# Kernel optimization log

Hardware: AMD Instinct MI355X
Metric: run time of the kernel (lower is better)

## Reference

```python
import jax, jax.numpy as jnp
import numpy as np

DIM = 256
HEADS = 8
DIM_HEAD = 64
INNER = HEADS * DIM_HEAD           # 512
DPG = DIM // HEADS                 # 32 in-channels per group (grouped conv)
EPS = 1e-5


def setup_inputs() -> dict:
    key = jax.random.key(0)
    ks = jax.random.split(key, 7)
    b, p, k = 4, 1024, 32
    x = jax.random.normal(ks[0], (b, p, k, DIM), dtype=jnp.float32)
    # BatchNorm2d affine params (torch default init: gamma=1, beta=0)
    bn_gamma = jnp.ones((DIM,), jnp.float32)
    bn_beta = jnp.zeros((DIM,), jnp.float32)
    # grouped 1x1 conv weights: per head maps DPG -> DIM_HEAD, shape [H, DIM_HEAD, DPG]
    Wq = jax.random.normal(ks[1], (HEADS, DIM_HEAD, DPG), jnp.float32) * 0.02
    Wk = jax.random.normal(ks[2], (HEADS, DIM_HEAD, DPG), jnp.float32) * 0.02
    Wv = jax.random.normal(ks[3], (HEADS, DIM_HEAD, DPG), jnp.float32) * 0.02
    # output Linear: y = x @ Wout + bout, Wout [INNER, DIM]
    Wout = jax.random.normal(ks[4], (INNER, DIM), jnp.float32) * 0.02
    bout = jnp.zeros((DIM,), jnp.float32)
    return {"x": x, "bn_gamma": bn_gamma, "bn_beta": bn_beta,
            "Wq": Wq, "Wk": Wk, "Wv": Wv, "Wout": Wout, "bout": bout}


def reference(x, bn_gamma, bn_beta, Wq, Wk, Wv, Wout, bout):
    b, p, k, d = x.shape
    scale = DIM_HEAD ** (-0.5)
    # BatchNorm2d in training mode: per-channel batch stats over (b, p, k)
    mean = jnp.mean(x, axis=(0, 1, 2))
    var = jnp.var(x, axis=(0, 1, 2))           # biased variance (torch BN normalization)
    xn = (x - mean) * jax.lax.rsqrt(var + EPS) * bn_gamma + bn_beta
    # grouped 1x1 conv projections: split channels into HEADS groups of DPG
    xg = xn.reshape(b, p, k, HEADS, DPG)       # [b,p,k,h,c]
    q = jnp.einsum('bpkhc,hoc->bphko', xg, Wq)  # [b,p,h,k,dim_head]
    kk = jnp.einsum('bpkhc,hoc->bphko', xg, Wk)
    v = jnp.einsum('bpkhc,hoc->bphko', xg, Wv)
    # attention over neighbors within each point
    dots = jnp.einsum('bphid,bphjd->bphij', q, kk) * scale  # [b,p,h,k,k]
    attn = jax.nn.softmax(dots, axis=-1)
    out = jnp.einsum('bphij,bphjd->bphid', attn, v)         # [b,p,h,k,dim_head]
    out = out.transpose(0, 1, 3, 2, 4).reshape(b, p, k, INNER)  # b p k (h d)
    return out @ Wout + bout                   # [b,p,k,dim]
```

## Files before the change

### kernel.cpp

```cpp
#include <hip/hip_runtime.h>
#include <hip/hip_bf16.h>

#define DIM    256
#define HEADS  8
#define DH     64
#define DPG    32
#define KNB    32
#define INNER  512
#define EPS    1e-5f

#define WS_SUMB 0
#define WS_SSQB 1024
#define WS_WF   2048
#define WS_QB   26624
#define WS_WT   28160

typedef float f32x4  __attribute__((ext_vector_type(4)));
typedef short bf16x8 __attribute__((ext_vector_type(8)));

__device__ __forceinline__ unsigned short f2bf(float f){
    unsigned u = __float_as_uint(f);
    u += 0x7fffu + ((u >> 16) & 1u);
    return (unsigned short)(u >> 16);
}
__device__ __forceinline__ unsigned packbf(float a, float b){
    union { __hip_bfloat162 h; unsigned u; } c;
    c.h = __float22bfloat162_rn(make_float2(a, b));
    return c.u;
}
__device__ __forceinline__ bf16x8 pack8(f32x4 a, f32x4 b){
    union { unsigned u[4]; bf16x8 v; } r;
    r.u[0] = packbf(a[0], a[1]); r.u[1] = packbf(a[2], a[3]);
    r.u[2] = packbf(b[0], b[1]); r.u[3] = packbf(b[2], b[3]);
    return r.v;
}

#define QKSWZ(row, col) ((row) * 64 + ((col) ^ ((((row) ^ ((row) >> 2)) & 7) << 3)))
#define AOSWZ(row, col) ((row) * 512 + ((col) ^ (((row) & 7) << 3)))

__global__ __launch_bounds__(256) void bn_stats_k(const f32x4* __restrict__ x4,
                                                  float* __restrict__ ws, int n4) {
    __shared__ f32x4 rs[4][64], rss[4][64];
    const int tid = blockIdx.x * 256 + threadIdx.x;
    const int stride = gridDim.x * 256;
    f32x4 s  = {0.f, 0.f, 0.f, 0.f};
    f32x4 ss = {0.f, 0.f, 0.f, 0.f};
    int f = tid;
    const int nloop = n4 / (4 * stride);
    for (int i = 0; i < nloop; ++i) {
        f32x4 v0 = x4[f];
        f32x4 v1 = x4[f + stride];
        f32x4 v2 = x4[f + 2 * stride];
        f32x4 v3 = x4[f + 3 * stride];
        f += 4 * stride;
        s += v0; ss += v0 * v0;
        s += v1; ss += v1 * v1;
        s += v2; ss += v2 * v2;
        s += v3; ss += v3 * v3;
    }
    for (; f < n4; f += stride) { f32x4 v = x4[f]; s += v; ss += v * v; }
    int c4 = threadIdx.x & 63, wv = threadIdx.x >> 6;
    rs[wv][c4] = s; rss[wv][c4] = ss;
    __syncthreads();
    const float* rsf  = (const float*)rs;
    const float* rssf = (const float*)rss;
    int ch = threadIdx.x;
    float S = rsf[ch]  + rsf[256 + ch]  + rsf[512 + ch]  + rsf[768 + ch];
    float Q = rssf[ch] + rssf[256 + ch] + rssf[512 + ch] + rssf[768 + ch];
    int bank = (blockIdx.x & 3) * 256;
    atomicAdd(&ws[WS_SUMB + bank + ch], S);
    atomicAdd(&ws[WS_SSQB + bank + ch], Q);
}

__global__ __launch_bounds__(256) void wt_k(const float* __restrict__ Wout, float* __restrict__ ws) {
    __shared__ unsigned short tile[64][65];
    const int k0 = blockIdx.x * 64, n0 = blockIdx.y * 64;
    const int t = threadIdx.x;
    #pragma unroll
    for (int i = 0; i < 16; ++i) {
        int e = t + 256 * i;
        int kk = e >> 6, nn = e & 63;
        tile[kk][nn] = f2bf(Wout[(k0 + kk) * DIM + n0 + nn]);
    }
    __syncthreads();
    unsigned short* wt = (unsigned short*)(ws + WS_WT);
    #pragma unroll
    for (int i = 0; i < 2; ++i) {
        int f = t + 256 * i;
        int nn = f >> 3, kc = f & 7;
        union { unsigned short s[8]; uint4 u; } pk;
        #pragma unroll
        for (int j = 0; j < 8; ++j) pk.s[j] = tile[kc * 8 + j][nn];
        *(uint4*)(wt + (size_t)(n0 + nn) * INNER + k0 + kc * 8) = pk.u;
    }
}

__global__ __launch_bounds__(256) void fold_k(const float* __restrict__ Wq,
                                              const float* __restrict__ Wk,
                                              const float* __restrict__ Wv,
                                              const float* __restrict__ gam,
                                              const float* __restrict__ bet,
                                              float* __restrict__ ws, float inv_n) {
    __shared__ float wl[64][33];
    __shared__ float scs[DPG], shs[DPG];
    const int m = blockIdx.x, h = blockIdx.y, t = threadIdx.x;
    const float* W = (m == 0 ? Wq : (m == 1 ? Wk : Wv)) + h * DH * DPG;
    if (t < DPG) {
        int c = h * DPG + t;
        float S = ws[WS_SUMB + c] + ws[WS_SUMB + 256 + c] + ws[WS_SUMB + 512 + c] + ws[WS_SUMB + 768 + c];
        float Q = ws[WS_SSQB + c] + ws[WS_SSQB + 256 + c] + ws[WS_SSQB + 512 + c] + ws[WS_SSQB + 768 + c];
        float mean = S * inv_n;
        float var  = Q * inv_n - mean * mean;
        float sc   = gam[c] * rsqrtf(var + EPS);
        scs[t] = sc;
        shs[t] = bet[c] - mean * sc;
    }
    #pragma unroll
    for (int i = 0; i < 8; ++i) {
        int e = t + 256 * i;
        wl[e >> 5][e & 31] = W[e];
    }
    __syncthreads();
    const float qsc = (m == 0) ? 0.125f : 1.f;
    unsigned short* wf = (unsigned short*)(ws + WS_WF) + (m * HEADS + h) * DH * DPG;
    {
        int o = t >> 2, c0 = (t & 3) * 8;
        union { unsigned short s[8]; uint4 u; } pk;
        #pragma unroll
        for (int j = 0; j < 8; ++j) pk.s[j] = f2bf(wl[o][c0 + j] * scs[c0 + j] * qsc);
        *(uint4*)(wf + o * DPG + c0) = pk.u;
    }
    if (t < DH) {
        float bias = 0.f;
        #pragma unroll
        for (int c = 0; c < DPG; ++c) bias += shs[c] * wl[t][c];
        ws[WS_QB + (m * HEADS + h) * DH + t] = bias * qsc;
    }
}

__global__ __launch_bounds__(256, 5) void attn_fused(const float* __restrict__ x,
                                                     const float* __restrict__ ws,
                                                     const float* __restrict__ bout,
                                                     float* __restrict__ out) {
    __shared__ __align__(16) unsigned short lds[16384];

    const int t = threadIdx.x;
    const int w = t >> 6, L = t & 63;
    const int lr = L & 15, g = L >> 4;
    const long long rb = (long long)blockIdx.x * KNB;

    unsigned short* qsm = lds + w * 2048;
    unsigned short* ksm = lds + 8192 + w * 2048;
    unsigned short* psm = qsm;
    unsigned short* vtm = ksm;
    const unsigned short* wfb = (const unsigned short*)(ws + WS_WF);
    const unsigned short* WT  = (const unsigned short*)(ws + WS_WT);

    bf16x8 xa[2][2];
    #pragma unroll
    for (int hs = 0; hs < 2; ++hs)
        #pragma unroll
        for (int it = 0; it < 2; ++it) {
            const float* xp = x + (rb + it * 16 + lr) * DIM + (w + hs * 4) * DPG + g * 8;
            xa[hs][it] = pack8(*(const f32x4*)xp, *(const f32x4*)(xp + 4));
        }

    f32x4 av[2][2][4];

    #pragma unroll
    for (int hs = 0; hs < 2; ++hs) {
        const int h = w + hs * 4;

        #pragma unroll
        for (int m = 0; m < 2; ++m) {
            unsigned short* dst = m ? ksm : qsm;
            #pragma unroll
            for (int ot = 0; ot < 4; ++ot) {
                const int o = ot * 16 + lr;
                bf16x8 wf = *(const bf16x8*)(wfb + ((m * HEADS + h) * DH + o) * DPG + g * 8);
                float bv = ws[WS_QB + (m * HEADS + h) * DH + o];
                #pragma unroll
                for (int it = 0; it < 2; ++it) {
                    f32x4 c = {bv, bv, bv, bv};
                    c = __builtin_amdgcn_mfma_f32_16x16x32_bf16(xa[hs][it], wf, c, 0, 0, 0);
                    unsigned u01 = packbf(c[0], c[1]);
                    unsigned u23 = packbf(c[2], c[3]);
                    const int r0 = it * 16 + g * 4;
                    dst[QKSWZ(r0 + 0, o)] = (unsigned short)u01;
                    dst[QKSWZ(r0 + 1, o)] = (unsigned short)(u01 >> 16);
                    dst[QKSWZ(r0 + 2, o)] = (unsigned short)u23;
                    dst[QKSWZ(r0 + 3, o)] = (unsigned short)(u23 >> 16);
                }
            }
        }

        f32x4 dt[2][2];
        #pragma unroll
        for (int it = 0; it < 2; ++it)
            #pragma unroll
            for (int jt = 0; jt < 2; ++jt) dt[it][jt] = (f32x4){0.f, 0.f, 0.f, 0.f};
        #pragma unroll
        for (int ksp = 0; ksp < 2; ++ksp) {
            bf16x8 qa[2], kb[2];
            #pragma unroll
            for (int it = 0; it < 2; ++it)
                qa[it] = *(const bf16x8*)(qsm + QKSWZ(it * 16 + lr, ksp * 32 + g * 8));
            #pragma unroll
            for (int jt = 0; jt < 2; ++jt)
                kb[jt] = *(const bf16x8*)(ksm + QKSWZ(jt * 16 + lr, ksp * 32 + g * 8));
            #pragma unroll
            for (int it = 0; it < 2; ++it)
                #pragma unroll
                for (int jt = 0; jt < 2; ++jt)
                    dt[it][jt] = __builtin_amdgcn_mfma_f32_16x16x32_bf16(qa[it], kb[jt], dt[it][jt], 0, 0, 0);
        }

        #pragma unroll
        for (int it = 0; it < 2; ++it)
            #pragma unroll
            for (int r = 0; r < 4; ++r) {
                float m0 = fmaxf(dt[it][0][r], dt[it][1][r]);
                m0 = fmaxf(m0, __shfl_xor(m0, 1, 64));
                m0 = fmaxf(m0, __shfl_xor(m0, 2, 64));
                m0 = fmaxf(m0, __shfl_xor(m0, 4, 64));
                m0 = fmaxf(m0, __shfl_xor(m0, 8, 64));
                float e0 = __expf(dt[it][0][r] - m0);
                float e1 = __expf(dt[it][1][r] - m0);
                float s = e0 + e1;
                s += __shfl_xor(s, 1, 64);
                s += __shfl_xor(s, 2, 64);
                s += __shfl_xor(s, 4, 64);
                s += __shfl_xor(s, 8, 64);
                float inv = 1.f / s;
                int row = it * 16 + g * 4 + r;
                unsigned up = packbf(e0 * inv, e1 * inv);
                psm[QKSWZ(row, lr)]      = (unsigned short)up;
                psm[QKSWZ(row, lr + 16)] = (unsigned short)(up >> 16);
            }

        #pragma unroll
        for (int ot = 0; ot < 4; ++ot) {
            const int o = ot * 16 + lr;
            bf16x8 wf = *(const bf16x8*)(wfb + ((2 * HEADS + h) * DH + o) * DPG + g * 8);
            float bv = ws[WS_QB + (2 * HEADS + h) * DH + o];
            #pragma unroll
            for (int it = 0; it < 2; ++it) {
                f32x4 c = {bv, bv, bv, bv};
                c = __builtin_amdgcn_mfma_f32_16x16x32_bf16(xa[hs][it], wf, c, 0, 0, 0);
                uint2 u;
                u.x = packbf(c[0], c[1]);
                u.y = packbf(c[2], c[3]);
                *(uint2*)(vtm + QKSWZ(o & 31, (o >> 5) * 32 + it * 16 + g * 4)) = u;
            }
        }

        #pragma unroll
        for (int it = 0; it < 2; ++it) {
            bf16x8 pa = *(const bf16x8*)(psm + QKSWZ(it * 16 + lr, g * 8));
            #pragma unroll
            for (int ot = 0; ot < 4; ++ot) {
                bf16x8 vb = *(const bf16x8*)(vtm + QKSWZ((ot & 1) * 16 + lr, (ot >> 1) * 32 + g * 8));
                f32x4 c = {0.f, 0.f, 0.f, 0.f};
                av[hs][it][ot] = __builtin_amdgcn_mfma_f32_16x16x32_bf16(pa, vb, c, 0, 0, 0);
            }
        }
    }

    __syncthreads();
    unsigned short* aos = lds;
    #pragma unroll
    for (int hs = 0; hs < 2; ++hs)
        #pragma unroll
        for (int it = 0; it < 2; ++it)
            #pragma unroll
            for (int ot = 0; ot < 4; ++ot)
                #pragma unroll
                for (int r = 0; r < 4; ++r)
                    aos[AOSWZ(it * 16 + g * 4 + r, (w + hs * 4) * 64 + ot * 16 + lr)]
                        = f2bf(av[hs][it][ot][r]);
    __syncthreads();

    f32x4 oacc[2][4];
    #pragma unroll
    for (int n4 = 0; n4 < 4; ++n4) {
        float bv = bout[(w * 4 + n4) * 16 + lr];
        oacc[0][n4] = (f32x4){bv, bv, bv, bv};
        oacc[1][n4] = (f32x4){bv, bv, bv, bv};
    }
    #pragma unroll 4
    for (int ksp = 0; ksp < 16; ++ksp) {
        bf16x8 a0 = *(const bf16x8*)(aos + AOSWZ(lr, ksp * 32 + g * 8));
        bf16x8 a1 = *(const bf16x8*)(aos + AOSWZ(16 + lr, ksp * 32 + g * 8));
        #pragma unroll
        for (int n4 = 0; n4 < 4; ++n4) {
            const int n = (w * 4 + n4) * 16 + lr;
            bf16x8 bvv = *(const bf16x8*)(WT + (size_t)n * INNER + ksp * 32 + g * 8);
            oacc[0][n4] = __builtin_amdgcn_mfma_f32_16x16x32_bf16(a0, bvv, oacc[0][n4], 0, 0, 0);
            oacc[1][n4] = __builtin_amdgcn_mfma_f32_16x16x32_bf16(a1, bvv, oacc[1][n4], 0, 0, 0);
        }
    }
    #pragma unroll
    for (int it = 0; it < 2; ++it)
        #pragma unroll
        for (int n4 = 0; n4 < 4; ++n4)
            #pragma unroll
            for (int r = 0; r < 4; ++r)
                out[(rb + it * 16 + g * 4 + r) * DIM + (w * 4 + n4) * 16 + lr] = oacc[it][n4][r];
}

extern "C" void kernel_launch(void* const* d_in, const int* in_sizes, int n_in,
                              void* d_out, int out_size, void* d_ws, size_t ws_size,
                              hipStream_t stream) {
    const float* x  = (const float*)d_in[0];
    const float* g  = (const float*)d_in[1];
    const float* b  = (const float*)d_in[2];
    const float* wq = (const float*)d_in[3];
    const float* wk = (const float*)d_in[4];
    const float* wv = (const float*)d_in[5];
    const float* wo = (const float*)d_in[6];
    const float* bo = (const float*)d_in[7];
    float* ws = (float*)d_ws;

    int rows = in_sizes[0] / DIM;
    int npts = rows / KNB;

    hipMemsetAsync(d_ws, 0, 8192, stream);
    wt_k<<<dim3(INNER / 64, DIM / 64), 256, 0, stream>>>(wo, ws);
    bn_stats_k<<<1024, 256, 0, stream>>>((const f32x4*)x, ws, rows * (DIM / 4));
    fold_k<<<dim3(3, HEADS), 256, 0, stream>>>(wq, wk, wv, g, b, ws, 1.0f / (float)rows);
    attn_fused<<<npts, 256, 0, stream>>>(x, ws, bo, (float*)d_out);
}
```

Before: 482.0 us.

## Merge weight transpose and BN stats kernels; pack AV outputs to bf16 early

```diff
diff --git a/kernel.cpp b/kernel.cpp
--- a/kernel.cpp
+++ b/kernel.cpp
@@ -38,60 +38,64 @@
 #define QKSWZ(row, col) ((row) * 64 + ((col) ^ ((((row) ^ ((row) >> 2)) & 7) << 3)))
 #define AOSWZ(row, col) ((row) * 512 + ((col) ^ (((row) & 7) << 3)))
 
-__global__ __launch_bounds__(256) void bn_stats_k(const f32x4* __restrict__ x4,
-                                                  float* __restrict__ ws, int n4) {
-    __shared__ f32x4 rs[4][64], rss[4][64];
-    const int tid = blockIdx.x * 256 + threadIdx.x;
-    const int stride = gridDim.x * 256;
-    f32x4 s  = {0.f, 0.f, 0.f, 0.f};
-    f32x4 ss = {0.f, 0.f, 0.f, 0.f};
-    int f = tid;
-    const int nloop = n4 / (4 * stride);
-    for (int i = 0; i < nloop; ++i) {
-        f32x4 v0 = x4[f];
-        f32x4 v1 = x4[f + stride];
-        f32x4 v2 = x4[f + 2 * stride];
-        f32x4 v3 = x4[f + 3 * stride];
-        f += 4 * stride;
-        s += v0; ss += v0 * v0;
-        s += v1; ss += v1 * v1;
-        s += v2; ss += v2 * v2;
-        s += v3; ss += v3 * v3;
-    }
-    for (; f < n4; f += stride) { f32x4 v = x4[f]; s += v; ss += v * v; }
-    int c4 = threadIdx.x & 63, wv = threadIdx.x >> 6;
-    rs[wv][c4] = s; rss[wv][c4] = ss;
-    __syncthreads();
-    const float* rsf  = (const float*)rs;
-    const float* rssf = (const float*)rss;
-    int ch = threadIdx.x;
-    float S = rsf[ch]  + rsf[256 + ch]  + rsf[512 + ch]  + rsf[768 + ch];
-    float Q = rssf[ch] + rssf[256 + ch] + rssf[512 + ch] + rssf[768 + ch];
-    int bank = (blockIdx.x & 3) * 256;
-    atomicAdd(&ws[WS_SUMB + bank + ch], S);
-    atomicAdd(&ws[WS_SSQB + bank + ch], Q);
-}
-
-__global__ __launch_bounds__(256) void wt_k(const float* __restrict__ Wout, float* __restrict__ ws) {
-    __shared__ unsigned short tile[64][65];
-    const int k0 = blockIdx.x * 64, n0 = blockIdx.y * 64;
+__global__ __launch_bounds__(256) void prep_k(const float* __restrict__ Wout,
+                                              const f32x4* __restrict__ x4,
+                                              float* __restrict__ ws, int n4) {
+    __shared__ __align__(16) unsigned char smem[8448];
     const int t = threadIdx.x;
-    #pragma unroll
-    for (int i = 0; i < 16; ++i) {
-        int e = t + 256 * i;
-        int kk = e >> 6, nn = e & 63;
-        tile[kk][nn] = f2bf(Wout[(k0 + kk) * DIM + n0 + nn]);
-    }
-    __syncthreads();
-    unsigned short* wt = (unsigned short*)(ws + WS_WT);
-    #pragma unroll
-    for (int i = 0; i < 2; ++i) {
-        int f = t + 256 * i;
-        int nn = f >> 3, kc = f & 7;
-        union { unsigned short s[8]; uint4 u; } pk;
-        #pragma unroll
-        for (int j = 0; j < 8; ++j) pk.s[j] = tile[kc * 8 + j][nn];
-        *(uint4*)(wt + (size_t)(n0 + nn) * INNER + k0 + kc * 8) = pk.u;
+    if (blockIdx.x < 32) {
+        unsigned short (*tile)[65] = (unsigned short (*)[65])smem;
+        const int k0 = (blockIdx.x & 7) * 64, n0 = (blockIdx.x >> 3) * 64;
+        #pragma unroll
+        for (int i = 0; i < 16; ++i) {
+            int e = t + 256 * i;
+            int kk = e >> 6, nn = e & 63;
+            tile[kk][nn] = f2bf(Wout[(k0 + kk) * DIM + n0 + nn]);
+        }
+        __syncthreads();
+        unsigned short* wt = (unsigned short*)(ws + WS_WT);
+        #pragma unroll
+        for (int i = 0; i < 2; ++i) {
+            int f = t + 256 * i;
+            int nn = f >> 3, kc = f & 7;
+            union { unsigned short s[8]; uint4 u; } pk;
+            #pragma unroll
+            for (int j = 0; j < 8; ++j) pk.s[j] = tile[kc * 8 + j][nn];
+            *(uint4*)(wt + (size_t)(n0 + nn) * INNER + k0 + kc * 8) = pk.u;
+        }
+    } else {
+        f32x4 (*rs)[64]  = (f32x4 (*)[64])smem;
+        f32x4 (*rss)[64] = (f32x4 (*)[64])(smem + 4096);
+        const int bid = blockIdx.x - 32;
+        const int tid = bid * 256 + t;
+        const int stride = 1024 * 256;
+        f32x4 s  = {0.f, 0.f, 0.f, 0.f};
+        f32x4 ss = {0.f, 0.f, 0.f, 0.f};
+        int f = tid;
+        const int nloop = n4 / (4 * stride);
+        for (int i = 0; i < nloop; ++i) {
+            f32x4 v0 = x4[f];
+            f32x4 v1 = x4[f + stride];
+            f32x4 v2 = x4[f + 2 * stride];
+            f32x4 v3 = x4[f + 3 * stride];
+            f += 4 * stride;
+            s += v0; ss += v0 * v0;
+            s += v1; ss += v1 * v1;
+            s += v2; ss += v2 * v2;
+            s += v3; ss += v3 * v3;
+        }
+        for (; f < n4; f += stride) { f32x4 v = x4[f]; s += v; ss += v * v; }
+        int c4 = t & 63, wv = t >> 6;
+        rs[wv][c4] = s; rss[wv][c4] = ss;
+        __syncthreads();
+        const float* rsf  = (const float*)rs;
+        const float* rssf = (const float*)rss;
+        int ch = t;
+        float S = rsf[ch]  + rsf[256 + ch]  + rsf[512 + ch]  + rsf[768 + ch];
+        float Q = rssf[ch] + rssf[256 + ch] + rssf[512 + ch] + rssf[768 + ch];
+        int bank = (bid & 3) * 256;
+        atomicAdd(&ws[WS_SUMB + bank + ch], S);
+        atomicAdd(&ws[WS_SSQB + bank + ch], Q);
     }
 }
 
@@ -138,7 +142,7 @@
     }
 }
 
-__global__ __launch_bounds__(256, 5) void attn_fused(const float* __restrict__ x,
+__global__ __launch_bounds__(256, 4) void attn_fused(const float* __restrict__ x,
                                                      const float* __restrict__ ws,
                                                      const float* __restrict__ bout,
                                                      float* __restrict__ out) {
@@ -165,7 +169,7 @@
             xa[hs][it] = pack8(*(const f32x4*)xp, *(const f32x4*)(xp + 4));
         }
 
-    f32x4 av[2][2][4];
+    unsigned av_pk[2][2][4][2];
 
     #pragma unroll
     for (int hs = 0; hs < 2; ++hs) {
@@ -261,7 +265,9 @@
             for (int ot = 0; ot < 4; ++ot) {
                 bf16x8 vb = *(const bf16x8*)(vtm + QKSWZ((ot & 1) * 16 + lr, (ot >> 1) * 32 + g * 8));
                 f32x4 c = {0.f, 0.f, 0.f, 0.f};
-                av[hs][it][ot] = __builtin_amdgcn_mfma_f32_16x16x32_bf16(pa, vb, c, 0, 0, 0);
+                c = __builtin_amdgcn_mfma_f32_16x16x32_bf16(pa, vb, c, 0, 0, 0);
+                av_pk[hs][it][ot][0] = packbf(c[0], c[1]);
+                av_pk[hs][it][ot][1] = packbf(c[2], c[3]);
             }
         }
     }
@@ -273,11 +279,16 @@
         #pragma unroll
         for (int it = 0; it < 2; ++it)
             #pragma unroll
-            for (int ot = 0; ot < 4; ++ot)
-                #pragma unroll
-                for (int r = 0; r < 4; ++r)
-                    aos[AOSWZ(it * 16 + g * 4 + r, (w + hs * 4) * 64 + ot * 16 + lr)]
-                        = f2bf(av[hs][it][ot][r]);
+            for (int ot = 0; ot < 4; ++ot) {
+                unsigned u0 = av_pk[hs][it][ot][0];
+                unsigned u1 = av_pk[hs][it][ot][1];
+                const int colb = (w + hs * 4) * 64 + ot * 16 + lr;
+                const int r0 = it * 16 + g * 4;
+                aos[AOSWZ(r0 + 0, colb)] = (unsigned short)u0;
+                aos[AOSWZ(r0 + 1, colb)] = (unsigned short)(u0 >> 16);
+                aos[AOSWZ(r0 + 2, colb)] = (unsigned short)u1;
+                aos[AOSWZ(r0 + 3, colb)] = (unsigned short)(u1 >> 16);
+            }
     __syncthreads();
 
     f32x4 oacc[2][4];
@@ -325,8 +336,7 @@
     int npts = rows / KNB;
 
     hipMemsetAsync(d_ws, 0, 8192, stream);
-    wt_k<<<dim3(INNER / 64, DIM / 64), 256, 0, stream>>>(wo, ws);
-    bn_stats_k<<<1024, 256, 0, stream>>>((const f32x4*)x, ws, rows * (DIM / 4));
+    prep_k<<<1056, 256, 0, stream>>>(wo, (const f32x4*)x, ws, rows * (DIM / 4));
     fold_k<<<dim3(3, HEADS), 256, 0, stream>>>(wq, wk, wv, g, b, ws, 1.0f / (float)rows);
     attn_fused<<<npts, 256, 0, stream>>>(x, ws, bo, (float*)d_out);
 }
```

After: 424.1 us. 12.0% less time.
